# Optimization experiments

Measured on AMD Instinct MI355X. Metric: run time of the kernel, lower is better.

Reference implementation:

```python
import jax, jax.numpy as jnp
import numpy as np

IC = 8      # inter_channels = in_channels // 2
K = 5       # top-k
EPS = 1e-5  # BatchNorm eps


def _conv(x, w, b, stride, pad):
    y = jax.lax.conv_general_dilated(
        x, w, (stride, stride), [(pad, pad), (pad, pad)],
        dimension_numbers=('NCHW', 'OIHW', 'NCHW'))
    return y + b[None, :, None, None]


def _maxpool2(x):
    return jax.lax.reduce_window(x, -jnp.inf, jax.lax.max,
                                 (1, 1, 2, 2), (1, 1, 2, 2), 'VALID')


def _up2(x):
    return jnp.repeat(jnp.repeat(x, 2, axis=2), 2, axis=3)


def setup_inputs() -> dict:
    key = jax.random.key(0)
    ks = jax.random.split(key, 12)
    C = 16
    x_ms = jax.random.normal(ks[0], (1, C, 96, 96), jnp.float32)
    hp_pan = jax.random.normal(ks[1], (1, C, 192, 192), jnp.float32)
    x_pan = jax.random.normal(ks[2], (1, C, 192, 192), jnp.float32)
    s = 0.05
    return {
        'x_ms': x_ms, 'hp_pan': hp_pan, 'x_pan': x_pan,
        'g_w': jax.random.normal(ks[3], (IC, C, 1, 1), jnp.float32) * s,
        'g_b': jax.random.normal(ks[4], (IC,), jnp.float32) * s,
        'theta_w': jax.random.normal(ks[5], (IC, C, 3, 3), jnp.float32) * s,
        'theta_b': jax.random.normal(ks[6], (IC,), jnp.float32) * s,
        'phi_w': jax.random.normal(ks[7], (IC, C, 3, 3), jnp.float32) * s,
        'phi_b': jax.random.normal(ks[8], (IC,), jnp.float32) * s,
        'W_w': jax.random.normal(ks[9], (C, IC, 1, 1), jnp.float32) * s,
        'W_b': jax.random.normal(ks[10], (C,), jnp.float32) * s,
        'bn_gamma': jax.random.normal(ks[11], (C,), jnp.float32) * s + 1.0,
        'bn_beta': jnp.zeros((C,), jnp.float32),
    }


def reference(x_ms, hp_pan, x_pan, g_w, g_b, theta_w, theta_b,
              phi_w, phi_b, W_w, W_b, bn_gamma, bn_beta):
    B, _, H, W = x_ms.shape
    # g: 1x1 conv + maxpool2 on hp_pan -> (B, M, IC)
    g_x = _maxpool2(_conv(hp_pan, g_w, g_b, 1, 0))
    g_x = g_x.reshape(B, IC, -1).transpose(0, 2, 1)
    # theta: 3x3 s2 conv + up2 on x_ms -> (B, N, IC), N = H*W
    th = _up2(_conv(x_ms, theta_w, theta_b, 2, 1))
    th = th.reshape(B, IC, -1).transpose(0, 2, 1)
    # phi: 3x3 s2 conv + maxpool2 + up2 on x_pan -> (B, IC, M)
    ph = _up2(_maxpool2(_conv(x_pan, phi_w, phi_b, 2, 1)))
    ph = ph.reshape(B, IC, -1)
    # dense similarity (B, N, M)
    f = jnp.einsum('bnc,bcm->bnm', th, ph)
    scores, idx = jax.lax.top_k(f, K)            # (B, N, K)
    scores = jax.nn.softmax(scores, axis=-1)
    # weighted matmul with V restricted to top-k columns (same math as
    # scatter-into-zeros followed by dense matmul, without the dense zeros)
    bi = jnp.arange(B)[:, None, None]
    g_sel = g_x[bi, idx]                          # (B, N, K, IC)
    y = jnp.einsum('bnk,bnkc->bnc', scores, g_sel)
    y = y.transpose(0, 2, 1).reshape(B, IC, H, W)
    wy = _conv(y, W_w, W_b, 1, 0)
    # BatchNorm2d (training-mode batch statistics)
    mean = wy.mean(axis=(0, 2, 3), keepdims=True)
    var = wy.var(axis=(0, 2, 3), keepdims=True)
    z = (wy - mean) * jax.lax.rsqrt(var + EPS)
    z = z * bn_gamma[None, :, None, None] + bn_beta[None, :, None, None]
    return (z, x_pan)
```

## Files before the change

### kernel.cpp

```cpp
#include <hip/hip_runtime.h>

#define IC 8
#define NC 2304
#define NF 9216
#define Z_ELEMS 147456
#define XPAN_ELEMS 589824

typedef unsigned int uint_t;

__global__ __launch_bounds__(256) void k1_prep(
    const float* __restrict__ xms,
    const float* __restrict__ hppan,
    const float* __restrict__ xpan,
    const float* __restrict__ gw, const float* __restrict__ gb,
    const float* __restrict__ thw, const float* __restrict__ thb,
    const float* __restrict__ phw, const float* __restrict__ phb,
    float* __restrict__ theta_c,
    float* __restrict__ phi_c,
    float* __restrict__ gmat,
    float* __restrict__ xpan_out)
{
    const int b = blockIdx.x;
    const int tid = threadIdx.x;

    if (b < 9) {
        int pix = b * 256 + tid;
        int r = pix / 48, c = pix % 48;
        int ir0 = 2 * r - 1, ic0 = 2 * c - 1;
        bool rok = (r > 0), cok = (c > 0);
        float acc[8];
        #pragma unroll
        for (int co = 0; co < 8; ++co) acc[co] = thb[co];
        #pragma unroll 4
        for (int ci = 0; ci < 16; ++ci) {
            const float* base = xms + ci * 9216;
            float xv[9];
            #pragma unroll
            for (int dr = 0; dr < 3; ++dr) {
                #pragma unroll
                for (int dc = 0; dc < 3; ++dc) {
                    bool ok = (dr > 0 || rok) && (dc > 0 || cok);
                    int off = (ir0 + dr) * 96 + (ic0 + dc);
                    float v = base[ok ? off : 0];
                    xv[dr * 3 + dc] = ok ? v : 0.0f;
                }
            }
            #pragma unroll
            for (int tap = 0; tap < 9; ++tap) {
                #pragma unroll
                for (int co = 0; co < 8; ++co)
                    acc[co] += thw[co * 144 + ci * 9 + tap] * xv[tap];
            }
        }
        #pragma unroll
        for (int co = 0; co < 8; ++co) theta_c[pix * 8 + co] = acc[co];
    } else if (b < 45) {
        int idx = (b - 9) * 256 + tid;
        int cp = idx >> 2, sp = idx & 3;
        int rc = cp / 48, cc = cp % 48;
        int r96 = 2 * rc + (sp >> 1), c96 = 2 * cc + (sp & 1);
        int ir0 = 2 * r96 - 1, ic0 = 2 * c96 - 1;
        bool rok = (r96 > 0), cok = (c96 > 0);
        float acc[8];
        #pragma unroll
        for (int co = 0; co < 8; ++co) acc[co] = 0.0f;
        #pragma unroll 4
        for (int ci = 0; ci < 16; ++ci) {
            const float* base = xpan + ci * 36864;
            float xv[9];
            #pragma unroll
            for (int dr = 0; dr < 3; ++dr) {
                #pragma unroll
                for (int dc = 0; dc < 3; ++dc) {
                    bool ok = (dr > 0 || rok) && (dc > 0 || cok);
                    int off = (ir0 + dr) * 192 + (ic0 + dc);
                    float v = base[ok ? off : 0];
                    xv[dr * 3 + dc] = ok ? v : 0.0f;
                }
            }
            #pragma unroll
            for (int tap = 0; tap < 9; ++tap) {
                #pragma unroll
                for (int co = 0; co < 8; ++co)
                    acc[co] += phw[co * 144 + ci * 9 + tap] * xv[tap];
            }
        }
        #pragma unroll
        for (int co = 0; co < 8; ++co) {
            float v = acc[co];
            v = fmaxf(v, __shfl_xor(v, 1));
            v = fmaxf(v, __shfl_xor(v, 2));
            if (sp == 0) phi_c[cp * 8 + co] = v + phb[co];
        }
    } else if (b < 189) {
        int idx = (b - 45) * 256 + tid;
        int op = idx >> 2, sp = idx & 3;
        int r = 2 * (op / 96) + (sp >> 1), c = 2 * (op % 96) + (sp & 1);
        const float* bp = hppan + r * 192 + c;
        float acc[8];
        #pragma unroll
        for (int co = 0; co < 8; ++co) acc[co] = 0.0f;
        #pragma unroll
        for (int ci = 0; ci < 16; ++ci) {
            float xv = bp[ci * 36864];
            #pragma unroll
            for (int co = 0; co < 8; ++co)
                acc[co] += gw[co * 16 + ci] * xv;
        }
        #pragma unroll
        for (int co = 0; co < 8; ++co) {
            float v = acc[co];
            v = fmaxf(v, __shfl_xor(v, 1));
            v = fmaxf(v, __shfl_xor(v, 2));
            if (sp == 0) gmat[op * 8 + co] = v + gb[co];
        }
    } else {
        int i = (b - 189) * 256 + tid;
        ((uint4*)xpan_out)[i] = ((const uint4*)xpan)[i];
    }
}

__global__ __launch_bounds__(256) void k2_attn(
    const float* __restrict__ theta_c, const float* __restrict__ phi_c,
    const float* __restrict__ gmat, float* __restrict__ y_c)
{
    __shared__ float4 ph4[NC * 2];
    const int tid = threadIdx.x;
    const float4* src = (const float4*)phi_c;
    #pragma unroll
    for (int j = 0; j < 18; ++j)
        ph4[tid + j * 256] = src[tid + j * 256];
    __syncthreads();

    const int wv = tid >> 6, lane = tid & 63;
    const int nc = __builtin_amdgcn_readfirstlane(blockIdx.x * 4 + wv);

    float th[8];
    #pragma unroll
    for (int j = 0; j < 8; ++j) th[j] = theta_c[nc * 8 + j];

    float v1 = -INFINITY, v2 = -INFINITY;
    int i1 = 0x7fffffff, i2 = 0x7fffffff;
    #pragma unroll 4
    for (int it = 0; it < 36; ++it) {
        int mc = lane + (it << 6);
        float4 a = ph4[mc * 2], bq = ph4[mc * 2 + 1];
        float v = th[0] * a.x + th[1] * a.y + th[2] * a.z + th[3] * a.w
                + th[4] * bq.x + th[5] * bq.y + th[6] * bq.z + th[7] * bq.w;
        if (v > v1)      { v2 = v1; i2 = i1; v1 = v; i1 = mc; }
        else if (v > v2) { v2 = v; i2 = mc; }
    }
    #pragma unroll
    for (int off = 1; off < 64; off <<= 1) {
        float ov1 = __shfl_xor(v1, off);
        int   oi1 = __shfl_xor(i1, off);
        float ov2 = __shfl_xor(v2, off);
        int   oi2 = __shfl_xor(i2, off);
        bool afirst = (v1 > ov1) || (v1 == ov1 && i1 < oi1);
        if (afirst) {
            bool t = (v2 > ov1) || (v2 == ov1 && i2 < oi1);
            v2 = t ? v2 : ov1; i2 = t ? i2 : oi1;
        } else {
            bool t = (ov2 > v1) || (ov2 == v1 && oi2 < i1);
            float nv2 = t ? ov2 : v1; int ni2 = t ? oi2 : i1;
            v1 = ov1; i1 = oi1; v2 = nv2; i2 = ni2;
        }
    }
    if (lane < 8) {
        int rc1 = i1 / 48, cc1 = i1 % 48;
        int m00 = (2 * rc1) * 96 + 2 * cc1;
        int rc2 = i2 / 48, cc2 = i2 % 48;
        int m2  = (2 * rc2) * 96 + 2 * cc2;
        float e = __expf(v2 - v1);
        float inv = 1.0f / (4.0f + e);
        float gs = gmat[m00 * 8 + lane] + gmat[(m00 + 1) * 8 + lane]
                 + gmat[(m00 + 96) * 8 + lane] + gmat[(m00 + 97) * 8 + lane];
        y_c[nc * 8 + lane] = inv * gs + (e * inv) * gmat[m2 * 8 + lane];
    }
}

__global__ __launch_bounds__(256) void k3_out(
    const float* __restrict__ y_c,
    const float* __restrict__ Ww, const float* __restrict__ Wb,
    const float* __restrict__ gamma, const float* __restrict__ beta,
    float* __restrict__ zout)
{
    const int co = blockIdx.x;
    const int tid = threadIdx.x;
    float w[8];
    #pragma unroll
    for (int j = 0; j < 8; ++j) w[j] = Ww[co * 8 + j];
    const float bias = Wb[co];

    float wy[9];
    float s = 0.f, s2 = 0.f;
    #pragma unroll
    for (int j = 0; j < 9; ++j) {
        int mc = tid + j * 256;
        const float4* p = (const float4*)(y_c + mc * 8);
        float4 a = p[0], bq = p[1];
        float v = bias + w[0] * a.x + w[1] * a.y + w[2] * a.z + w[3] * a.w
                       + w[4] * bq.x + w[5] * bq.y + w[6] * bq.z + w[7] * bq.w;
        wy[j] = v; s += v; s2 += v * v;
    }
    #pragma unroll
    for (int off = 32; off; off >>= 1) {
        s  += __shfl_down(s, off);
        s2 += __shfl_down(s2, off);
    }
    __shared__ float ps[4], ps2[4];
    __shared__ float sc_s, sh_s;
    int wv = tid >> 6, lane = tid & 63;
    if (lane == 0) { ps[wv] = s; ps2[wv] = s2; }
    __syncthreads();
    if (tid == 0) {
        float S  = ps[0] + ps[1] + ps[2] + ps[3];
        float S2 = ps2[0] + ps2[1] + ps2[2] + ps2[3];
        float mean = S * (1.0f / 2304.0f);
        float var  = S2 * (1.0f / 2304.0f) - mean * mean;
        float rsig = 1.0f / sqrtf(var + 1e-5f);
        float gm = gamma[co], be = beta[co];
        sc_s = gm * rsig;
        sh_s = be - mean * gm * rsig;
    }
    __syncthreads();
    float sc = sc_s, sh = sh_s;
    #pragma unroll
    for (int j = 0; j < 9; ++j) {
        int mc = tid + j * 256;
        int rc = mc / 48, cc = mc % 48;
        float zv = wy[j] * sc + sh;
        float2 zz = make_float2(zv, zv);
        int base = co * 9216 + (2 * rc) * 96 + 2 * cc;
        *(float2*)(zout + base) = zz;
        *(float2*)(zout + base + 96) = zz;
    }
}

extern "C" void kernel_launch(void* const* d_in, const int* in_sizes, int n_in,
                              void* d_out, int out_size, void* d_ws, size_t ws_size,
                              hipStream_t stream) {
    const float* xms   = (const float*)d_in[0];
    const float* hppan = (const float*)d_in[1];
    const float* xpan  = (const float*)d_in[2];
    const float* gw    = (const float*)d_in[3];
    const float* gb    = (const float*)d_in[4];
    const float* thw   = (const float*)d_in[5];
    const float* thb   = (const float*)d_in[6];
    const float* phw   = (const float*)d_in[7];
    const float* phb   = (const float*)d_in[8];
    const float* Ww    = (const float*)d_in[9];
    const float* Wb    = (const float*)d_in[10];
    const float* gam   = (const float*)d_in[11];
    const float* bet   = (const float*)d_in[12];

    float* zout     = (float*)d_out;
    float* xpan_out = zout + Z_ELEMS;

    float* theta_c = (float*)d_ws;
    float* phi_c   = theta_c + NC * IC;
    float* gmat    = phi_c + NC * IC;
    float* y_c     = gmat + NF * IC;

    k1_prep<<<765, 256, 0, stream>>>(xms, hppan, xpan, gw, gb, thw, thb,
                                     phw, phb, theta_c, phi_c, gmat, xpan_out);
    k2_attn<<<576, 256, 0, stream>>>(theta_c, phi_c, gmat, y_c);
    k3_out<<<16, 256, 0, stream>>>(y_c, Ww, Wb, gam, bet, zout);
}
```

Measured before the change: 115.0 us.

## Split phi columns across waves and drop shared-memory staging in attention kernel

Each wave of the attention block now scans a quarter of the phi columns straight from global memory for all four query rows, instead of every block copying the whole 73 KB phi matrix into LDS and each wave scanning all columns for one row. Per-wave top-2 candidates are merged through a small shared array and a final cross-wave reduction. This removes the large per-block LDS fill and its occupancy limit, at the cost of more registers per thread, a second reduction stage, and global/L2 reads of phi.

```diff
diff --git a/kernel.cpp b/kernel.cpp
--- a/kernel.cpp
+++ b/kernel.cpp
@@ -124,58 +124,95 @@
     const float* __restrict__ theta_c, const float* __restrict__ phi_c,
     const float* __restrict__ gmat, float* __restrict__ y_c)
 {
-    __shared__ float4 ph4[NC * 2];
     const int tid = threadIdx.x;
-    const float4* src = (const float4*)phi_c;
-    #pragma unroll
-    for (int j = 0; j < 18; ++j)
-        ph4[tid + j * 256] = src[tid + j * 256];
+    const int wv = tid >> 6, lane = tid & 63;
+    const int nc0 = blockIdx.x * 4;
+
+    float th[4][8];
+    #pragma unroll
+    for (int r = 0; r < 4; ++r)
+        #pragma unroll
+        for (int j = 0; j < 8; ++j)
+            th[r][j] = theta_c[(nc0 + r) * 8 + j];
+
+    float v1[4], v2[4];
+    int i1[4], i2[4];
+    #pragma unroll
+    for (int r = 0; r < 4; ++r) {
+        v1[r] = -INFINITY; v2[r] = -INFINITY;
+        i1[r] = 0x7fffffff; i2[r] = 0x7fffffff;
+    }
+
+    #pragma unroll
+    for (int it = 0; it < 9; ++it) {
+        int mc = lane + ((it * 4 + wv) << 6);
+        const float4* p = (const float4*)(phi_c + mc * 8);
+        float4 a = p[0], bq = p[1];
+        #pragma unroll
+        for (int r = 0; r < 4; ++r) {
+            float v = th[r][0] * a.x + th[r][1] * a.y + th[r][2] * a.z + th[r][3] * a.w
+                    + th[r][4] * bq.x + th[r][5] * bq.y + th[r][6] * bq.z + th[r][7] * bq.w;
+            if (v > v1[r])      { v2[r] = v1[r]; i2[r] = i1[r]; v1[r] = v; i1[r] = mc; }
+            else if (v > v2[r]) { v2[r] = v; i2[r] = mc; }
+        }
+    }
+
+    #pragma unroll
+    for (int r = 0; r < 4; ++r) {
+        #pragma unroll
+        for (int off = 1; off < 64; off <<= 1) {
+            float ov1 = __shfl_xor(v1[r], off);
+            int   oi1 = __shfl_xor(i1[r], off);
+            float ov2 = __shfl_xor(v2[r], off);
+            int   oi2 = __shfl_xor(i2[r], off);
+            bool afirst = (v1[r] > ov1) || (v1[r] == ov1 && i1[r] < oi1);
+            if (afirst) {
+                bool t = (v2[r] > ov1) || (v2[r] == ov1 && i2[r] < oi1);
+                v2[r] = t ? v2[r] : ov1; i2[r] = t ? i2[r] : oi1;
+            } else {
+                bool t = (ov2 > v1[r]) || (ov2 == v1[r] && oi2 < i1[r]);
+                float nv2 = t ? ov2 : v1[r]; int ni2 = t ? oi2 : i1[r];
+                v1[r] = ov1; i1[r] = oi1; v2[r] = nv2; i2[r] = ni2;
+            }
+        }
+    }
+
+    __shared__ float cv1[4][4], cv2[4][4];
+    __shared__ int   ci1[4][4], ci2[4][4];
+    if (lane == 0) {
+        #pragma unroll
+        for (int r = 0; r < 4; ++r) {
+            cv1[wv][r] = v1[r]; ci1[wv][r] = i1[r];
+            cv2[wv][r] = v2[r]; ci2[wv][r] = i2[r];
+        }
+    }
     __syncthreads();
 
-    const int wv = tid >> 6, lane = tid & 63;
-    const int nc = __builtin_amdgcn_readfirstlane(blockIdx.x * 4 + wv);
-
-    float th[8];
-    #pragma unroll
-    for (int j = 0; j < 8; ++j) th[j] = theta_c[nc * 8 + j];
-
-    float v1 = -INFINITY, v2 = -INFINITY;
-    int i1 = 0x7fffffff, i2 = 0x7fffffff;
-    #pragma unroll 4
-    for (int it = 0; it < 36; ++it) {
-        int mc = lane + (it << 6);
-        float4 a = ph4[mc * 2], bq = ph4[mc * 2 + 1];
-        float v = th[0] * a.x + th[1] * a.y + th[2] * a.z + th[3] * a.w
-                + th[4] * bq.x + th[5] * bq.y + th[6] * bq.z + th[7] * bq.w;
-        if (v > v1)      { v2 = v1; i2 = i1; v1 = v; i1 = mc; }
-        else if (v > v2) { v2 = v; i2 = mc; }
-    }
-    #pragma unroll
-    for (int off = 1; off < 64; off <<= 1) {
-        float ov1 = __shfl_xor(v1, off);
-        int   oi1 = __shfl_xor(i1, off);
-        float ov2 = __shfl_xor(v2, off);
-        int   oi2 = __shfl_xor(i2, off);
-        bool afirst = (v1 > ov1) || (v1 == ov1 && i1 < oi1);
-        if (afirst) {
-            bool t = (v2 > ov1) || (v2 == ov1 && i2 < oi1);
-            v2 = t ? v2 : ov1; i2 = t ? i2 : oi1;
-        } else {
-            bool t = (ov2 > v1) || (ov2 == v1 && oi2 < i1);
-            float nv2 = t ? ov2 : v1; int ni2 = t ? oi2 : i1;
-            v1 = ov1; i1 = oi1; v2 = nv2; i2 = ni2;
-        }
-    }
-    if (lane < 8) {
-        int rc1 = i1 / 48, cc1 = i1 % 48;
+    if (tid < 32) {
+        int r = tid >> 3, ch = tid & 7;
+        float m1 = -INFINITY, m2 = -INFINITY;
+        int j1 = 0x7fffffff, j2 = 0x7fffffff;
+        #pragma unroll
+        for (int w = 0; w < 4; ++w) {
+            #pragma unroll
+            for (int s = 0; s < 2; ++s) {
+                float v = s ? cv2[w][r] : cv1[w][r];
+                int   i = s ? ci2[w][r] : ci1[w][r];
+                bool b1 = (v > m1) || (v == m1 && i < j1);
+                bool b2 = (v > m2) || (v == m2 && i < j2);
+                if (b1)      { m2 = m1; j2 = j1; m1 = v; j1 = i; }
+                else if (b2) { m2 = v; j2 = i; }
+            }
+        }
+        int rc1 = j1 / 48, cc1 = j1 % 48;
         int m00 = (2 * rc1) * 96 + 2 * cc1;
-        int rc2 = i2 / 48, cc2 = i2 % 48;
-        int m2  = (2 * rc2) * 96 + 2 * cc2;
-        float e = __expf(v2 - v1);
+        int rc2 = j2 / 48, cc2 = j2 % 48;
+        int mm2 = (2 * rc2) * 96 + 2 * cc2;
+        float e = __expf(m2 - m1);
         float inv = 1.0f / (4.0f + e);
-        float gs = gmat[m00 * 8 + lane] + gmat[(m00 + 1) * 8 + lane]
-                 + gmat[(m00 + 96) * 8 + lane] + gmat[(m00 + 97) * 8 + lane];
-        y_c[nc * 8 + lane] = inv * gs + (e * inv) * gmat[m2 * 8 + lane];
+        float gs = gmat[m00 * 8 + ch] + gmat[(m00 + 1) * 8 + ch]
+                 + gmat[(m00 + 96) * 8 + ch] + gmat[(m00 + 97) * 8 + ch];
+        y_c[(nc0 + r) * 8 + ch] = inv * gs + (e * inv) * gmat[mm2 * 8 + ch];
     }
 }
 
```

After: 118.8 us. +3.2%, slower.
